# Optimization experiments

Measured on AMD Instinct MI355X. Metric: run time of the kernel, lower is better.

## Reference

```python
import jax, jax.numpy as jnp
import numpy as np
from jax import lax

B, N = 2048, 8192


def setup_inputs() -> dict:
    key = jax.random.key(0)
    k1, k2 = jax.random.split(key)
    # alpha in [0, 0.3) keeps the tridiagonal system diagonally dominant in fp32
    alpha = 0.3 * jax.random.uniform(k1, (B, N), dtype=jnp.float32)
    f = jax.random.normal(k2, (N,), dtype=jnp.float32)
    return {"alpha": alpha, "f": f}


def _thomas(a, b, c, f):
    """Batched Thomas solve. a: (B,N-1) sub, b: (B,N) diag, c: (B,N-1) super, f: (B,N)."""
    Bn = b.shape[0]
    a_p = jnp.pad(a, ((0, 0), (1, 0)))  # a_0 := 0
    c_p = jnp.pad(c, ((0, 0), (0, 1)))  # c_{N-1} := 0

    def fwd(carry, x):
        cp_prev, dp_prev = carry
        ai, bi, ci, fi = x
        denom = bi - ai * cp_prev
        cp = ci / denom
        dp = (fi - ai * dp_prev) / denom
        return (cp, dp), (cp, dp)

    zeros = jnp.zeros((Bn,), dtype=b.dtype)
    _, (cps, dps) = lax.scan(fwd, (zeros, zeros), (a_p.T, b.T, c_p.T, f.T))

    def bwd(u_next, x):
        cp, dp = x
        u = dp - cp * u_next
        return u, u

    _, us = lax.scan(bwd, zeros, (cps, dps), reverse=True)
    return us.T  # (B, N)


def reference(alpha, f):
    # Tridiagonal matrix A(alpha)
    a = alpha[:, :-1] ** 2                      # subdiagonal
    b = 1.0 + alpha ** 3                        # diagonal
    c = alpha[:, 1:] ** 2 + 2.0 * alpha[:, 1:]  # superdiagonal
    f_b = jnp.broadcast_to(f, alpha.shape)      # (B, N)
    return _thomas(a, b, c, f_b)
```

## Files before the change

kernel.cpp:

```cpp
#include <hip/hip_runtime.h>


#define NN 8192
#define TB 1024
#define CH 8
#define NWAVE (TB/64)

__device__ __forceinline__ float frcp(float x) { return __builtin_amdgcn_rcpf(x); }

#define COMPOSE(p2,q2,r2,s2,t2,u2,v2, p1,q1,r1,s1,t1,u1,v1, P,Q,R,S,T,U,V) \
    { P = (p2)*(p1) + (q2)*(u1);                                           \
      Q = (p2)*(q1) + (q2)*(v1);                                           \
      R = (r2)*(p1) + (s2)*(r1) + (t2)*(u1);                               \
      S = (s2)*(s1);                                                       \
      T = (r2)*(q1) + (s2)*(t1) + (t2)*(v1);                               \
      U = (u2)*(p1) + (v2)*(u1);                                           \
      V = (u2)*(q1) + (v2)*(v1); }

__global__ __launch_bounds__(TB, 8)
void thomas_scan_kernel(const float* __restrict__ alpha,
                        const float* __restrict__ fvec,
                        float* __restrict__ out)
{
    __shared__ float wtot[NWAVE][7];
    __shared__ float btot[NWAVE][2];

    const int t    = threadIdx.x;
    const int lane = t & 63;
    const int wid  = t >> 6;
    const int row  = blockIdx.x;
    const float* __restrict__ arow = alpha + (size_t)row * NN;
    const int base = t * CH;

    float va[CH], vf[CH];
    {
        const float4* a4 = reinterpret_cast<const float4*>(arow + base);
        const float4* f4 = reinterpret_cast<const float4*>(fvec + base);
        #pragma unroll
        for (int k = 0; k < CH / 4; ++k) {
            float4 x = a4[k];
            va[4*k+0]=x.x; va[4*k+1]=x.y; va[4*k+2]=x.z; va[4*k+3]=x.w;
            float4 y = f4[k];
            vf[4*k+0]=y.x; vf[4*k+1]=y.y; vf[4*k+2]=y.z; vf[4*k+3]=y.w;
        }
    }
    const float aL = (t > 0)      ? arow[base - 1]  : 0.0f;
    const float aR = (t < TB - 1) ? arow[base + CH] : 0.0f;

    float p=1.f, q=0.f, r=0.f, s=1.f, tt=0.f, u=0.f, v=1.f;
    #pragma unroll
    for (int k = 0; k < CH; ++k) {
        const float am1 = (k == 0)      ? aL : va[k-1];
        const float ap1 = (k == CH - 1) ? aR : va[k+1];
        const float ai = am1 * am1;
        const float bi = 1.0f + va[k]*va[k]*va[k];
        const float ci = ap1 * (ap1 + 2.0f);
        const float fi = vf[k];
        const float np = ci*u,        nq = ci*v;
        const float nr = fi*u - ai*r, ns = -ai*s, nt = fi*v - ai*tt;
        const float nu = bi*u - ai*p, nv = bi*v - ai*q;
        p=np; q=nq; r=nr; s=ns; tt=nt; u=nu; v=nv;
    }
    { const float inv = frcp(v); p*=inv; q*=inv; r*=inv; s*=inv; tt*=inv; u*=inv; v=1.0f; }

    #pragma unroll
    for (int off = 1; off < 64; off <<= 1) {
        const float p1 = __shfl_up(p, off);
        const float q1 = __shfl_up(q, off);
        const float r1 = __shfl_up(r, off);
        const float s1 = __shfl_up(s, off);
        const float t1 = __shfl_up(tt, off);
        const float u1 = __shfl_up(u, off);
        const float v1 = __shfl_up(v, off);
        if (lane >= off) {
            float np,nq,nr,ns,nt,nu,nv;
            COMPOSE(p,q,r,s,tt,u,v, p1,q1,r1,s1,t1,u1,v1, np,nq,nr,ns,nt,nu,nv);
            p=np; q=nq; r=nr; s=ns; tt=nt; u=nu; v=nv;
        }
    }
    if (lane == 63) {
        wtot[wid][0]=p; wtot[wid][1]=q; wtot[wid][2]=r; wtot[wid][3]=s;
        wtot[wid][4]=tt; wtot[wid][5]=u; wtot[wid][6]=v;
    }
    __syncthreads();

    float ep=__shfl_up(p,1), eq=__shfl_up(q,1), er=__shfl_up(r,1),
          es=__shfl_up(s,1), et=__shfl_up(tt,1), eu=__shfl_up(u,1), ev=__shfl_up(v,1);
    if (lane == 0) { ep=1.f; eq=0.f; er=0.f; es=1.f; et=0.f; eu=0.f; ev=1.f; }

    float Pp=1.f, Pq=0.f, Pr=0.f, Ps=1.f, Pt=0.f, Pu=0.f, Pv=1.f;
    for (int w = 0; w < wid; ++w) {
        const float p1=wtot[w][0], q1=wtot[w][1], r1=wtot[w][2], s1=wtot[w][3],
                    t1=wtot[w][4], u1=wtot[w][5], v1=wtot[w][6];
        float np,nq,nr,ns,nt,nu,nv;
        COMPOSE(p1,q1,r1,s1,t1,u1,v1, Pp,Pq,Pr,Ps,Pt,Pu,Pv, np,nq,nr,ns,nt,nu,nv);
        Pp=np; Pq=nq; Pr=nr; Ps=ns; Pt=nt; Pu=nu; Pv=nv;
    }
    float cp, dp;
    {
        const float nq = ep*Pq + eq*Pv;
        const float nt = er*Pq + es*Pt + et*Pv;
        const float nv = eu*Pq + ev*Pv;
        const float inv = frcp(nv);
        cp = nq*inv; dp = nt*inv;
    }

    float cpv[CH], dpv[CH];
    #pragma unroll
    for (int k = 0; k < CH; ++k) {
        const float am1 = (k == 0)      ? aL : va[k-1];
        const float ap1 = (k == CH - 1) ? aR : va[k+1];
        const float ai = am1 * am1;
        const float bi = 1.0f + va[k]*va[k]*va[k];
        const float ci = ap1 * (ap1 + 2.0f);
        const float rd = frcp(bi - ai*cp);
        cp = ci * rd;
        dp = (vf[k] - ai*dp) * rd;
        cpv[k] = cp; dpv[k] = dp;
    }

    float A = 1.0f, Bb = 0.0f;
    #pragma unroll
    for (int k = CH - 1; k >= 0; --k) {
        Bb = dpv[k] - cpv[k]*Bb;
        A  = -cpv[k]*A;
    }
    #pragma unroll
    for (int off = 1; off < 64; off <<= 1) {
        const float A1 = __shfl_down(A, off);
        const float B1 = __shfl_down(Bb, off);
        if (lane < 64 - off) { Bb = A*B1 + Bb; A = A*A1; }
    }
    if (lane == 0) { btot[wid][0] = A; btot[wid][1] = Bb; }
    __syncthreads();

    float eA = __shfl_down(A, 1), eB = __shfl_down(Bb, 1);
    if (lane == 63) { eA = 1.0f; eB = 0.0f; }
    float SA = 1.0f, SB = 0.0f;
    for (int w = NWAVE - 1; w > wid; --w) {
        const float A1 = btot[w][0], B1 = btot[w][1];
        SB = A1*SB + B1;
        SA = A1*SA;
    }
    const float u_in = eA*SB + eB;

    float uv[CH];
    float un = u_in;
    #pragma unroll
    for (int k = CH - 1; k >= 0; --k) {
        un = dpv[k] - cpv[k]*un;
        uv[k] = un;
    }
    float4* o4 = reinterpret_cast<float4*>(out + (size_t)row * NN + base);
    #pragma unroll
    for (int k = 0; k < CH / 4; ++k) {
        o4[k] = make_float4(uv[4*k+0], uv[4*k+1], uv[4*k+2], uv[4*k+3]);
    }
}

extern "C" void kernel_launch(void* const* d_in, const int* in_sizes, int n_in,
                              void* d_out, int out_size, void* d_ws, size_t ws_size,
                              hipStream_t stream) {
    const float* alpha = (const float*)d_in[0];
    const float* fvec  = (const float*)d_in[1];
    float* out = (float*)d_out;
    const int nrows = out_size / NN;
    thomas_scan_kernel<<<nrows, TB, 0, stream>>>(alpha, fvec, out);
}
```

Before: 129.7 us.

## Split forward scan into 2x2 Möbius scan for cp and affine scan for dp

Replaces the single 7-element matrix scan over the forward sweep with two scans. The first is a 2x2 projective scan that computes only the c' recurrence. The second is a 2-element affine scan for d', which runs once the c' denominators are known. Shuffle and FMA work per step drops, and the a/b/c coefficients are precomputed once into registers. The cost is one extra block-level scan stage with another __syncthreads and more live registers per thread.

```diff
diff --git a/kernel.cpp b/kernel.cpp
--- a/kernel.cpp
+++ b/kernel.cpp
@@ -8,22 +8,14 @@
 
 __device__ __forceinline__ float frcp(float x) { return __builtin_amdgcn_rcpf(x); }
 
-#define COMPOSE(p2,q2,r2,s2,t2,u2,v2, p1,q1,r1,s1,t1,u1,v1, P,Q,R,S,T,U,V) \
-    { P = (p2)*(p1) + (q2)*(u1);                                           \
-      Q = (p2)*(q1) + (q2)*(v1);                                           \
-      R = (r2)*(p1) + (s2)*(r1) + (t2)*(u1);                               \
-      S = (s2)*(s1);                                                       \
-      T = (r2)*(q1) + (s2)*(t1) + (t2)*(v1);                               \
-      U = (u2)*(p1) + (v2)*(u1);                                           \
-      V = (u2)*(q1) + (v2)*(v1); }
-
 __global__ __launch_bounds__(TB, 8)
-void thomas_scan_kernel(const float* __restrict__ alpha,
-                        const float* __restrict__ fvec,
-                        float* __restrict__ out)
+void thomas_kernel(const float* __restrict__ alpha,
+                   const float* __restrict__ fvec,
+                   float* __restrict__ out)
 {
-    __shared__ float wtot[NWAVE][7];
-    __shared__ float btot[NWAVE][2];
+    __shared__ float wq[NWAVE][4];
+    __shared__ float wd[NWAVE][2];
+    __shared__ float wb[NWAVE][2];
 
     const int t    = threadIdx.x;
     const int lane = t & 63;
@@ -32,8 +24,9 @@
     const float* __restrict__ arow = alpha + (size_t)row * NN;
     const int base = t * CH;
 
-    float va[CH], vf[CH];
+    float ai[CH], bi[CH], ci[CH], vf[CH];
     {
+        float va[CH];
         const float4* a4 = reinterpret_cast<const float4*>(arow + base);
         const float4* f4 = reinterpret_cast<const float4*>(fvec + base);
         #pragma unroll
@@ -43,104 +36,123 @@
             float4 y = f4[k];
             vf[4*k+0]=y.x; vf[4*k+1]=y.y; vf[4*k+2]=y.z; vf[4*k+3]=y.w;
         }
+        const float aL = (t > 0)      ? arow[base - 1]  : 0.0f;
+        const float aR = (t < TB - 1) ? arow[base + CH] : 0.0f;
+        #pragma unroll
+        for (int k = 0; k < CH; ++k) {
+            const float am1 = (k == 0)      ? aL : va[k-1];
+            const float ap1 = (k == CH - 1) ? aR : va[k+1];
+            ai[k] = am1 * am1;
+            bi[k] = 1.0f + va[k]*va[k]*va[k];
+            ci[k] = ap1 * (ap1 + 2.0f);
+        }
     }
-    const float aL = (t > 0)      ? arow[base - 1]  : 0.0f;
-    const float aR = (t < TB - 1) ? arow[base + CH] : 0.0f;
 
-    float p=1.f, q=0.f, r=0.f, s=1.f, tt=0.f, u=0.f, v=1.f;
+    float p = 1.f, q = 0.f, u = 0.f, v = 1.f;
     #pragma unroll
     for (int k = 0; k < CH; ++k) {
-        const float am1 = (k == 0)      ? aL : va[k-1];
-        const float ap1 = (k == CH - 1) ? aR : va[k+1];
-        const float ai = am1 * am1;
-        const float bi = 1.0f + va[k]*va[k]*va[k];
-        const float ci = ap1 * (ap1 + 2.0f);
-        const float fi = vf[k];
-        const float np = ci*u,        nq = ci*v;
-        const float nr = fi*u - ai*r, ns = -ai*s, nt = fi*v - ai*tt;
-        const float nu = bi*u - ai*p, nv = bi*v - ai*q;
-        p=np; q=nq; r=nr; s=ns; tt=nt; u=nu; v=nv;
+        const float np = ci[k]*u;
+        const float nq = ci[k]*v;
+        const float nu = bi[k]*u - ai[k]*p;
+        const float nv = bi[k]*v - ai[k]*q;
+        p = np; q = nq; u = nu; v = nv;
     }
-    { const float inv = frcp(v); p*=inv; q*=inv; r*=inv; s*=inv; tt*=inv; u*=inv; v=1.0f; }
+    { const float inv = frcp(v); p*=inv; q*=inv; u*=inv; v = 1.0f; }
 
     #pragma unroll
     for (int off = 1; off < 64; off <<= 1) {
         const float p1 = __shfl_up(p, off);
         const float q1 = __shfl_up(q, off);
-        const float r1 = __shfl_up(r, off);
-        const float s1 = __shfl_up(s, off);
-        const float t1 = __shfl_up(tt, off);
         const float u1 = __shfl_up(u, off);
         const float v1 = __shfl_up(v, off);
         if (lane >= off) {
-            float np,nq,nr,ns,nt,nu,nv;
-            COMPOSE(p,q,r,s,tt,u,v, p1,q1,r1,s1,t1,u1,v1, np,nq,nr,ns,nt,nu,nv);
-            p=np; q=nq; r=nr; s=ns; tt=nt; u=nu; v=nv;
+            const float np = p*p1 + q*u1;
+            const float nq = p*q1 + q*v1;
+            const float nu = u*p1 + v*u1;
+            const float nv = u*q1 + v*v1;
+            p = np; q = nq; u = nu; v = nv;
         }
     }
-    if (lane == 63) {
-        wtot[wid][0]=p; wtot[wid][1]=q; wtot[wid][2]=r; wtot[wid][3]=s;
-        wtot[wid][4]=tt; wtot[wid][5]=u; wtot[wid][6]=v;
-    }
+    if (lane == 63) { wq[wid][0]=p; wq[wid][1]=q; wq[wid][2]=u; wq[wid][3]=v; }
     __syncthreads();
 
-    float ep=__shfl_up(p,1), eq=__shfl_up(q,1), er=__shfl_up(r,1),
-          es=__shfl_up(s,1), et=__shfl_up(tt,1), eu=__shfl_up(u,1), ev=__shfl_up(v,1);
-    if (lane == 0) { ep=1.f; eq=0.f; er=0.f; es=1.f; et=0.f; eu=0.f; ev=1.f; }
+    float ep=__shfl_up(p,1), eq=__shfl_up(q,1), eu=__shfl_up(u,1), ev=__shfl_up(v,1);
+    if (lane == 0) { ep=1.f; eq=0.f; eu=0.f; ev=1.f; }
 
-    float Pp=1.f, Pq=0.f, Pr=0.f, Ps=1.f, Pt=0.f, Pu=0.f, Pv=1.f;
+    float Pp=1.f, Pq=0.f, Pu=0.f, Pv=1.f;
     for (int w = 0; w < wid; ++w) {
-        const float p1=wtot[w][0], q1=wtot[w][1], r1=wtot[w][2], s1=wtot[w][3],
-                    t1=wtot[w][4], u1=wtot[w][5], v1=wtot[w][6];
-        float np,nq,nr,ns,nt,nu,nv;
-        COMPOSE(p1,q1,r1,s1,t1,u1,v1, Pp,Pq,Pr,Ps,Pt,Pu,Pv, np,nq,nr,ns,nt,nu,nv);
-        Pp=np; Pq=nq; Pr=nr; Ps=ns; Pt=nt; Pu=nu; Pv=nv;
+        const float p1=wq[w][0], q1=wq[w][1], u1=wq[w][2], v1=wq[w][3];
+        const float np = p1*Pp + q1*Pu;
+        const float nq = p1*Pq + q1*Pv;
+        const float nu = u1*Pp + v1*Pu;
+        const float nv = u1*Pq + v1*Pv;
+        Pp=np; Pq=nq; Pu=nu; Pv=nv;
     }
-    float cp, dp;
+    float cp;
     {
-        const float nq = ep*Pq + eq*Pv;
-        const float nt = er*Pq + es*Pt + et*Pv;
-        const float nv = eu*Pq + ev*Pv;
-        const float inv = frcp(nv);
-        cp = nq*inv; dp = nt*inv;
+        const float cpP = Pq * frcp(Pv);
+        cp = (ep*cpP + eq) * frcp(eu*cpP + ev);
     }
 
-    float cpv[CH], dpv[CH];
+    float cpv[CH], rdv[CH];
+    float G = 1.f, H = 0.f;
     #pragma unroll
     for (int k = 0; k < CH; ++k) {
-        const float am1 = (k == 0)      ? aL : va[k-1];
-        const float ap1 = (k == CH - 1) ? aR : va[k+1];
-        const float ai = am1 * am1;
-        const float bi = 1.0f + va[k]*va[k]*va[k];
-        const float ci = ap1 * (ap1 + 2.0f);
-        const float rd = frcp(bi - ai*cp);
-        cp = ci * rd;
-        dp = (vf[k] - ai*dp) * rd;
-        cpv[k] = cp; dpv[k] = dp;
+        const float rd = frcp(bi[k] - ai[k]*cp);
+        cp = ci[k] * rd;
+        cpv[k] = cp; rdv[k] = rd;
+        H = (vf[k] - ai[k]*H) * rd;
+        G = -(ai[k]*rd) * G;
     }
 
-    float A = 1.0f, Bb = 0.0f;
+    #pragma unroll
+    for (int off = 1; off < 64; off <<= 1) {
+        const float G1 = __shfl_up(G, off);
+        const float H1 = __shfl_up(H, off);
+        if (lane >= off) { H = G*H1 + H; G = G*G1; }
+    }
+    if (lane == 63) { wd[wid][0] = G; wd[wid][1] = H; }
+    __syncthreads();
+
+    float eG = __shfl_up(G, 1), eH = __shfl_up(H, 1);
+    if (lane == 0) { eG = 1.f; eH = 0.f; }
+    float Pg = 1.f, Ph = 0.f;
+    for (int w = 0; w < wid; ++w) {
+        const float Gw = wd[w][0], Hw = wd[w][1];
+        Ph = Gw*Ph + Hw;
+        Pg = Gw*Pg;
+    }
+    float dp = eG*Ph + eH;
+
+    float dpv[CH];
+    #pragma unroll
+    for (int k = 0; k < CH; ++k) {
+        dp = (vf[k] - ai[k]*dp) * rdv[k];
+        dpv[k] = dp;
+    }
+    float A = 1.f, Bb = 0.f;
     #pragma unroll
     for (int k = CH - 1; k >= 0; --k) {
         Bb = dpv[k] - cpv[k]*Bb;
         A  = -cpv[k]*A;
     }
+
     #pragma unroll
     for (int off = 1; off < 64; off <<= 1) {
         const float A1 = __shfl_down(A, off);
         const float B1 = __shfl_down(Bb, off);
         if (lane < 64 - off) { Bb = A*B1 + Bb; A = A*A1; }
     }
-    if (lane == 0) { btot[wid][0] = A; btot[wid][1] = Bb; }
+    if (lane == 0) { wb[wid][0] = A; wb[wid][1] = Bb; }
     __syncthreads();
 
     float eA = __shfl_down(A, 1), eB = __shfl_down(Bb, 1);
-    if (lane == 63) { eA = 1.0f; eB = 0.0f; }
-    float SA = 1.0f, SB = 0.0f;
+    if (lane == 63) { eA = 1.f; eB = 0.f; }
+    float SA = 1.f, SB = 0.f;
     for (int w = NWAVE - 1; w > wid; --w) {
-        const float A1 = btot[w][0], B1 = btot[w][1];
-        SB = A1*SB + B1;
-        SA = A1*SA;
+        const float Aw = wb[w][0], Bw = wb[w][1];
+        SB = Aw*SB + Bw;
+        SA = Aw*SA;
     }
     const float u_in = eA*SB + eB;
 
@@ -165,5 +177,5 @@
     const float* fvec  = (const float*)d_in[1];
     float* out = (float*)d_out;
     const int nrows = out_size / NN;
-    thomas_scan_kernel<<<nrows, TB, 0, stream>>>(alpha, fvec, out);
+    thomas_kernel<<<nrows, TB, 0, stream>>>(alpha, fvec, out);
 }
```

Result: slower. 155.5 us (+20.0%).
